# Performance work log

Hardware: AMD Instinct MI355X
Metric: run time of the kernel (lower is better)

## Reference

```python
import jax, jax.numpy as jnp
import numpy as np

B, S, G = 128, 128, 2000          # batch, set_size, n_genes
NH, H, NLAT = 256, 4, 64          # n_hidden, n_heads, n_latent
HD = NH // H                      # head_dim = 64
NGAT = 2                          # n_gat_layers
LN_EPS = 1e-5


def _layer_norm(x, g, b):
    mu = jnp.mean(x, axis=-1, keepdims=True)
    var = jnp.var(x, axis=-1, keepdims=True)
    return (x - mu) * jax.lax.rsqrt(var + LN_EPS) * g + b


def setup_inputs() -> dict:
    key = jax.random.key(0)
    ks = jax.random.split(key, 12)
    x_set = jax.random.normal(ks[0], (B, S, G), dtype=jnp.float32)
    adj = jax.random.randint(ks[1], (B, S, S), 0, 2).astype(jnp.int32)
    # guarantee self-loops so no softmax row is fully masked
    adj = jnp.maximum(adj, jnp.eye(S, dtype=jnp.int32)[None])
    w = 0.02
    return {
        "x_set": x_set,
        "adj": adj,
        "W_in": jax.random.normal(ks[2], (G, NH), dtype=jnp.float32) * w,
        "b_in": jnp.zeros((NH,), jnp.float32),
        "ln_in_g": jnp.ones((NH,), jnp.float32),
        "ln_in_b": jnp.zeros((NH,), jnp.float32),
        "Wg": jax.random.normal(ks[3], (NGAT, NH, NH), dtype=jnp.float32) * w,
        "a_src": jax.random.normal(ks[4], (NGAT, H, HD), dtype=jnp.float32) * 0.1,
        "a_dst": jax.random.normal(ks[5], (NGAT, H, HD), dtype=jnp.float32) * 0.1,
        "a_edge": jax.random.normal(ks[6], (NGAT, H, HD), dtype=jnp.float32) * 0.1,
        "We": jax.random.normal(ks[7], (NGAT, NH, NH), dtype=jnp.float32) * w,
        "ln_g": jnp.ones((NGAT, NH), jnp.float32),
        "ln_b": jnp.zeros((NGAT, NH), jnp.float32),
        "Wz": jax.random.normal(ks[8], (NH, NLAT), dtype=jnp.float32) * w,
        "bz": jnp.zeros((NLAT,), jnp.float32),
    }


def reference(x_set, adj, W_in, b_in, ln_in_g, ln_in_b, Wg, a_src, a_dst,
              a_edge, We, ln_g, ln_b, Wz, bz):
    # input_proj: Linear -> LayerNorm -> GELU (dropout = identity in eval)
    h = jax.nn.gelu(_layer_norm(x_set @ W_in + b_in, ln_in_g, ln_in_b),
                    approximate=False)
    masked = (adj == 0)[..., None]                       # (B,S,S,1)
    for l in range(NGAT):
        hp = (h @ Wg[l]).reshape(B, S, H, HD)            # W(x) per head
        s_src = jnp.einsum('bshd,hd->bsh', hp, a_src[l])
        s_dst = jnp.einsum('bshd,hd->bsh', hp, a_dst[l])
        # edge features e_ij = h_i - h_j; edge_proj is linear (no bias), so
        # <proj(h_i - h_j), a_edge> = es_i - es_j  (exactly the original math,
        # without materializing the (B,S,S,NH) tensor)
        es = jnp.einsum('bshd,hd->bsh', (h @ We[l]).reshape(B, S, H, HD),
                        a_edge[l])
        logits = (s_src + es)[:, :, None, :] + (s_dst - es)[:, None, :, :]
        logits = jnp.where(logits >= 0, logits, 0.2 * logits)  # LeakyReLU(0.2)
        logits = jnp.where(masked, -jnp.inf, logits)
        attn = jax.nn.softmax(logits, axis=2)            # over neighbors j
        out = jnp.einsum('bijh,bjhd->bihd', attn, hp).reshape(B, S, NH)
        h = jax.nn.gelu(_layer_norm(out, ln_g[l], ln_b[l]), approximate=False)
    z_all = h @ Wz + bz                                  # (B,S,NLAT)
    return z_all
```

## Files before the change

### kernel.cpp

```cpp
#include <hip/hip_runtime.h>
#include <hip/hip_bf16.h>
#include <cstdint>
#include <cstddef>

#define BB   128
#define SS   128
#define GG   2000
#define NHID 256
#define NHEAD 4
#define HDIM 64
#define NLAT 64
#define KPAD 2048
#define NSPLIT 4
#define KSPLIT 512

typedef __attribute__((ext_vector_type(4))) float f32x4;
typedef __attribute__((ext_vector_type(8))) short short8;
typedef __attribute__((ext_vector_type(4))) short bfs4;
typedef __attribute__((ext_vector_type(8))) __bf16 bf8_t;

static __device__ __forceinline__ bf8_t as_bf8(short8 s){
  union { short8 s; bf8_t b; } u; u.s = s; return u.b;
}

static __device__ __forceinline__ unsigned short f2bf(float f){
  union { float f; unsigned u; } x; x.f = f;
  unsigned r = x.u + 0x7fffu + ((x.u >> 16) & 1u);
  return (unsigned short)(r >> 16);
}

#define GLOAD_LDS16(g, l) __builtin_amdgcn_global_load_lds( \
    (const __attribute__((address_space(1))) unsigned int*)(g), \
    (__attribute__((address_space(3))) unsigned int*)(l), 16, 0, 0)

__global__ __launch_bounds__(256) void k_transconv(
    const float* __restrict__ W, unsigned short* __restrict__ Wt,
    int K, int N, int Kpad)
{
  int idx = blockIdx.x * 256 + threadIdx.x;
  if (idx >= N * Kpad) return;
  int n = idx / Kpad, k = idx - n * Kpad;
  float v = (k < K) ? W[(size_t)k * N + n] : 0.f;
  Wt[idx] = f2bf(v);
}

__global__ __launch_bounds__(256) void k_adjpack(
    const int* __restrict__ adj, unsigned long long* __restrict__ abits)
{
  const int wid  = blockIdx.x * 4 + (threadIdx.x >> 6);
  const int lane = threadIdx.x & 63;
  int v = adj[(size_t)wid * 64 + lane];
  unsigned long long m = __ballot(v != 0);
  if (lane == 0) abits[wid] = m;
}

__global__ __launch_bounds__(256, 4) void k_gemm_in(
    const float* __restrict__ X,
    const unsigned short* __restrict__ Bt,
    float* __restrict__ Out)
{
  __shared__ __align__(16) unsigned short Ab[2][4][64][8];
  __shared__ __align__(16) unsigned short Bb[2][16][64][8];
  const int tid = threadIdx.x, l = tid & 63, w = tid >> 6;
  const int m0 = blockIdx.x * 64;
  const int kbase = blockIdx.y * KSPLIT;
  const int kvalid = (GG - kbase < KSPLIT) ? (GG - kbase) : KSPLIT;
  const int nsteps = 16;

  const int akg8 = (l >> 4) * 8;
  const float* aP = X + (size_t)(m0 + (l & 15) + 16 * w) * GG + kbase + akg8;
  const unsigned short* bB = Bt + (size_t)(l & 15) * KPAD + kbase + akg8;

  f32x4 acc[4][4];
#pragma unroll
  for (int i = 0; i < 4; ++i)
#pragma unroll
    for (int j = 0; j < 4; ++j) acc[i][j] = (f32x4)(0.f);

  auto stage_b = [&](int buf, int koff) {
#pragma unroll
    for (int q = 0; q < 4; ++q) {
      const int tile = w * 4 + q;
      GLOAD_LDS16(bB + (size_t)(16 * tile) * KPAD + koff, &Bb[buf][tile][0][0]);
    }
  };
  auto load_a = [&](int koff, f32x4& a0, f32x4& a1, bool& ok) {
    ok = (koff + akg8 < kvalid);
    const float* p = ok ? (aP + koff) : (aP - akg8);
    a0 = *(const f32x4*)p;
    a1 = *(const f32x4*)(p + 4);
  };
  auto write_a = [&](int buf, f32x4 a0, f32x4 a1, bool ok) {
    if (!ok) { a0 = (f32x4)(0.f); a1 = (f32x4)(0.f); }
    bf8_t v;
    v[0]=(__bf16)a0.x; v[1]=(__bf16)a0.y; v[2]=(__bf16)a0.z; v[3]=(__bf16)a0.w;
    v[4]=(__bf16)a1.x; v[5]=(__bf16)a1.y; v[6]=(__bf16)a1.z; v[7]=(__bf16)a1.w;
    *(bf8_t*)&Ab[buf][w][l][0] = v;
  };

  {
    f32x4 a0, a1; bool ok;
    load_a(0, a0, a1, ok);
    stage_b(0, 0);
    write_a(0, a0, a1, ok);
  }
  __syncthreads();

  for (int s = 0; s < nsteps; ++s) {
    const int cur = s & 1;
    f32x4 a0, a1; bool ok = false;
    const bool more = (s + 1 < nsteps);
    if (more) {
      load_a((s + 1) * 32, a0, a1, ok);
      stage_b(cur ^ 1, (s + 1) * 32);
    }
    short8 af[4], bfv[4];
#pragma unroll
    for (int i = 0; i < 4; ++i) af[i]  = *(const short8*)&Ab[cur][i][l][0];
#pragma unroll
    for (int j = 0; j < 4; ++j) bfv[j] = *(const short8*)&Bb[cur][4 * w + j][l][0];
#pragma unroll
    for (int i = 0; i < 4; ++i)
#pragma unroll
      for (int j = 0; j < 4; ++j)
        acc[i][j] = __builtin_amdgcn_mfma_f32_16x16x32_bf16(
            as_bf8(af[i]), as_bf8(bfv[j]), acc[i][j], 0, 0, 0);
    if (more) write_a(cur ^ 1, a0, a1, ok);
    __syncthreads();
  }

  float* outp = Out + (size_t)blockIdx.y * ((size_t)BB * SS * NHID);
  const int orow = m0 + ((l >> 4) << 2);
  const int ocol = (w << 6) + (l & 15);
#pragma unroll
  for (int i = 0; i < 4; ++i)
#pragma unroll
    for (int j = 0; j < 4; ++j) {
      const int row = orow + i * 16, col = ocol + j * 16;
#pragma unroll
      for (int r = 0; r < 4; ++r)
        outp[(size_t)(row + r) * NHID + col] = acc[i][j][r];
    }
}

__global__ __launch_bounds__(256, 2) void k_gemm_hp(
    const unsigned short* __restrict__ A,
    const unsigned short* __restrict__ Bt,
    unsigned short* __restrict__ hpT)
{
  __shared__ __align__(16) unsigned short Ab[2][4][64][8];
  __shared__ __align__(16) unsigned short Bb[2][8][64][8];
  const int tid = threadIdx.x, l = tid & 63, w = tid >> 6;
  const int m0 = blockIdx.x * 64, n0 = blockIdx.y * 128;

  const unsigned short* aB = A  + (size_t)(m0 + (l & 15)) * NHID + (l >> 4) * 8;
  const unsigned short* bB = Bt + (size_t)(n0 + (l & 15)) * NHID + (l >> 4) * 8;

  f32x4 acc[4][2];
#pragma unroll
  for (int i = 0; i < 4; ++i)
#pragma unroll
    for (int j = 0; j < 2; ++j) acc[i][j] = (f32x4)(0.f);

  auto stage = [&](int buf, int koff) {
#pragma unroll
    for (int q = 0; q < 3; ++q) {
      const int t = w * 3 + q;
      if (t < 4) {
        GLOAD_LDS16(aB + (size_t)(16 * t) * NHID + koff, &Ab[buf][t][0][0]);
      } else {
        GLOAD_LDS16(bB + (size_t)(16 * (t - 4)) * NHID + koff, &Bb[buf][t - 4][0][0]);
      }
    }
  };

  stage(0, 0);
  __syncthreads();

  for (int s = 0; s < 8; ++s) {
    const int cur = s & 1;
    if (s + 1 < 8) stage(cur ^ 1, (s + 1) * 32);
    short8 af[4], bfv[2];
#pragma unroll
    for (int i = 0; i < 4; ++i) af[i]  = *(const short8*)&Ab[cur][i][l][0];
#pragma unroll
    for (int j = 0; j < 2; ++j) bfv[j] = *(const short8*)&Bb[cur][2 * w + j][l][0];
#pragma unroll
    for (int i = 0; i < 4; ++i)
#pragma unroll
      for (int j = 0; j < 2; ++j)
        acc[i][j] = __builtin_amdgcn_mfma_f32_16x16x32_bf16(
            as_bf8(af[i]), as_bf8(bfv[j]), acc[i][j], 0, 0, 0);
    __syncthreads();
  }

  const int bidx = m0 >> 7;
  const int rb0  = (m0 & 127) + ((l >> 4) << 2);
  unsigned short* hb = hpT + (size_t)bidx * NHID * SS;
#pragma unroll
  for (int i = 0; i < 4; ++i)
#pragma unroll
    for (int j = 0; j < 2; ++j) {
      const int col = n0 + (2 * w + j) * 16 + (l & 15);
      bfs4 o;
#pragma unroll
      for (int r = 0; r < 4; ++r) o[r] = (short)f2bf(acc[i][j][r]);
      *(bfs4*)&hb[(size_t)col * SS + rb0 + i * 16] = o;
    }
}

__global__ __launch_bounds__(256) void k_ln_fuse(
    const float* __restrict__ X0, int nparts, size_t pstride,
    const float* __restrict__ bias, const float* __restrict__ g,
    const float* __restrict__ b, unsigned short* __restrict__ out_bf,
    float* __restrict__ out_f32, const float* __restrict__ u,
    float* __restrict__ c1, float* __restrict__ c2)
{
  const int tid = threadIdx.x, l = tid & 63, w = tid >> 6;
  const f32x4 gg = *(const f32x4*)(g + l * 4);
  const f32x4 bb = *(const f32x4*)(b + l * 4);
  f32x4 bias4 = (f32x4)(0.f);
  if (bias) bias4 = *(const f32x4*)(bias + l * 4);
  f32x4 u1v[4], u2v[4];
  if (u) {
#pragma unroll
    for (int t = 0; t < 4; ++t) {
      u1v[t] = *(const f32x4*)(u + (size_t)(4 * l + t) * 4);
      u2v[t] = *(const f32x4*)(u + 1024 + (size_t)(4 * l + t) * 4);
    }
  }
  for (int it = 0; it < 4; ++it) {
    const int row = blockIdx.x * 16 + w * 4 + it;
    f32x4 x = *(const f32x4*)(X0 + (size_t)row * NHID + l * 4);
    for (int p = 1; p < nparts; ++p) {
      f32x4 x1 = *(const f32x4*)(X0 + p * pstride + (size_t)row * NHID + l * 4);
      x.x += x1.x; x.y += x1.y; x.z += x1.z; x.w += x1.w;
    }
    x.x += bias4.x; x.y += bias4.y; x.z += bias4.z; x.w += bias4.w;
    float s  = x.x + x.y + x.z + x.w;
    float sq = x.x * x.x + x.y * x.y + x.z * x.z + x.w * x.w;
#pragma unroll
    for (int m = 1; m < 64; m <<= 1) { s += __shfl_xor(s, m); sq += __shfl_xor(sq, m); }
    const float mu   = s * (1.f / 256.f);
    const float var  = sq * (1.f / 256.f) - mu * mu;
    const float rstd = rsqrtf(var + 1e-5f);
    float y[4];
#pragma unroll
    for (int t = 0; t < 4; ++t) {
      float yy = (x[t] - mu) * rstd * gg[t] + bb[t];
      y[t] = 0.5f * yy * (1.f + erff(yy * 0.70710678118654752f));
    }
    if (out_bf) {
      bfs4 o;
#pragma unroll
      for (int t = 0; t < 4; ++t) o[t] = (short)f2bf(y[t]);
      *(bfs4*)(out_bf + (size_t)row * NHID + l * 4) = o;
    }
    if (out_f32) {
      f32x4 o; o.x = y[0]; o.y = y[1]; o.z = y[2]; o.w = y[3];
      *(f32x4*)(out_f32 + (size_t)row * NHID + l * 4) = o;
    }
    if (u) {
      float d1[4] = {0.f,0.f,0.f,0.f}, d2[4] = {0.f,0.f,0.f,0.f};
#pragma unroll
      for (int t = 0; t < 4; ++t)
#pragma unroll
        for (int h = 0; h < 4; ++h) {
          d1[h] += y[t] * u1v[t][h];
          d2[h] += y[t] * u2v[t][h];
        }
#pragma unroll
      for (int h = 0; h < 4; ++h) {
#pragma unroll
        for (int m = 1; m < 64; m <<= 1) {
          d1[h] += __shfl_xor(d1[h], m);
          d2[h] += __shfl_xor(d2[h], m);
        }
      }
      if (l == 0) {
#pragma unroll
        for (int h = 0; h < 4; ++h) {
          c1[(size_t)row * 4 + h] = d1[h];
          c2[(size_t)row * 4 + h] = d2[h];
        }
      }
    }
  }
}

__global__ __launch_bounds__(256, 1) void k_proj(
    const float* __restrict__ Wg, const float* __restrict__ We,
    const float* __restrict__ asrc, const float* __restrict__ adst,
    const float* __restrict__ aedge, float* __restrict__ u)
{
  const int lyr = blockIdx.x;
  const int k = threadIdx.x;
  const float* Wgl = Wg + (size_t)lyr * NHID * NHID;
  const float* Wel = We + (size_t)lyr * NHID * NHID;
  float* u1 = u + (size_t)lyr * 2048;
  float* u2 = u1 + 1024;
#pragma unroll
  for (int h = 0; h < 4; ++h) {
    float ss = 0.f, sd = 0.f, se = 0.f;
    const float* wg  = Wgl + k * NHID + h * 64;
    const float* we  = Wel + k * NHID + h * 64;
    const float* pas = asrc + lyr * NHEAD * HDIM + h * 64;
    const float* pad_ = adst + lyr * NHEAD * HDIM + h * 64;
    const float* pae = aedge + lyr * NHEAD * HDIM + h * 64;
#pragma unroll 4
    for (int d = 0; d < 64; ++d) {
      ss += wg[d] * pas[d];
      sd += wg[d] * pad_[d];
      se += we[d] * pae[d];
    }
    u1[k * 4 + h] = ss + se;
    u2[k * 4 + h] = sd - se;
  }
}

__global__ __launch_bounds__(256) void k_attn2(
    const unsigned short* __restrict__ hpT, const float* __restrict__ c1,
    const float* __restrict__ c2, const unsigned long long* __restrict__ abits,
    float* __restrict__ out)
{
  __shared__ __align__(16) unsigned short Pb[4][8][64][8];
  __shared__ __align__(16) unsigned short Vb[4][4][64][8];
  __shared__ float s1[128], s2[128];
  __shared__ float mbuf[2][128], sbuf[2][128], invsum[128];
  const int head = blockIdx.x, b = blockIdx.y;
  const int tid = threadIdx.x, w = tid >> 6, l = tid & 63;

  if (tid < 128) {
    const int m = b * SS + tid;
    s1[tid] = c1[m * 4 + head];
    s2[tid] = c2[m * 4 + head];
  }
  {
    const unsigned short* hb = hpT + ((size_t)b * NHID + head * 64) * SS;
#pragma unroll
    for (int q = 0; q < 4; ++q) {
      const int tile = w * 4 + q;
      const int kstep = tile >> 2, nt = tile & 3;
      const unsigned short* src =
          hb + (size_t)(nt * 16 + (l & 15)) * SS + kstep * 32 + (l >> 4) * 8;
      GLOAD_LDS16(src, &Vb[kstep][nt][0][0]);
    }
  }
  __syncthreads();

  const int i = tid & 127, half = tid >> 7;
  const float s1v = s1[i];
  const unsigned long long bits = abits[((size_t)b * SS + i) * 2 + half];

  float ma[4] = {-3.0e38f, -3.0e38f, -3.0e38f, -3.0e38f};
#pragma unroll
  for (int jl = 0; jl < 64; ++jl) {
    float x  = s1v + s2[half * 64 + jl];
    float lk = fmaxf(x, 0.2f * x);
    float xm = ((bits >> jl) & 1ull) ? lk : -3.0e38f;
    ma[jl & 3] = fmaxf(ma[jl & 3], xm);
  }
  mbuf[half][i] = fmaxf(fmaxf(ma[0], ma[1]), fmaxf(ma[2], ma[3]));
  __syncthreads();
  const float mrow = fmaxf(mbuf[0][i], mbuf[1][i]);

  float sa[4] = {0.f, 0.f, 0.f, 0.f};
#pragma unroll
  for (int grp = 0; grp < 8; ++grp) {
    short8 pv;
#pragma unroll
    for (int e = 0; e < 8; ++e) {
      const int jl = grp * 8 + e;
      float x  = s1v + s2[half * 64 + jl];
      float lk = fmaxf(x, 0.2f * x);
      float xm = ((bits >> jl) & 1ull) ? lk : -3.0e38f;
      float p  = exp2f((xm - mrow) * 1.4426950408889634f);
      sa[e & 3] += p;
      pv[e] = (short)f2bf(p);
    }
    const int j = half * 64 + grp * 8;
    const int kstep = j >> 5, g = (j >> 3) & 3;
    *(short8*)&Pb[kstep][i >> 4][(g << 4) | (i & 15)][0] = pv;
  }
  sbuf[half][i] = (sa[0] + sa[1]) + (sa[2] + sa[3]);
  __syncthreads();
  if (tid < 128) invsum[tid] = 1.f / (sbuf[0][tid] + sbuf[1][tid]);
  __syncthreads();

  f32x4 acc[2][4];
#pragma unroll
  for (int ii = 0; ii < 2; ++ii)
#pragma unroll
    for (int nt = 0; nt < 4; ++nt) acc[ii][nt] = (f32x4)(0.f);
#pragma unroll
  for (int kstep = 0; kstep < 4; ++kstep) {
    short8 bv[4];
#pragma unroll
    for (int nt = 0; nt < 4; ++nt) bv[nt] = *(const short8*)&Vb[kstep][nt][l][0];
#pragma unroll
    for (int ii = 0; ii < 2; ++ii) {
      short8 af = *(const short8*)&Pb[kstep][2 * w + ii][l][0];
#pragma unroll
      for (int nt = 0; nt < 4; ++nt)
        acc[ii][nt] = __builtin_amdgcn_mfma_f32_16x16x32_bf16(
            as_bf8(af), as_bf8(bv[nt]), acc[ii][nt], 0, 0, 0);
    }
  }

  float* ob = out + (size_t)(b * SS) * NHID + head * 64;
#pragma unroll
  for (int ii = 0; ii < 2; ++ii) {
    const int it = 2 * w + ii;
#pragma unroll
    for (int r = 0; r < 4; ++r) {
      const int row = it * 16 + (l >> 4) * 4 + r;
      const float inv = invsum[row];
#pragma unroll
      for (int nt = 0; nt < 4; ++nt)
        ob[(size_t)row * NHID + nt * 16 + (l & 15)] = acc[ii][nt][r] * inv;
    }
  }
}

__global__ __launch_bounds__(256, 1) void k_zgemm(
    const float* __restrict__ hmat, const float* __restrict__ Wz,
    const float* __restrict__ bz, float* __restrict__ Z)
{
  __shared__ __align__(16) float hrows[64 * 256];
  const int tid = threadIdx.x, w = tid >> 6, l = tid & 63;
  const int r0 = blockIdx.x * 64;
  const f32x4* src = (const f32x4*)(hmat + (size_t)r0 * NHID);
#pragma unroll
  for (int rep = 0; rep < 16; ++rep)
    ((f32x4*)hrows)[rep * 256 + tid] = src[rep * 256 + tid];
  __syncthreads();
  const float bzv = bz[l];
  const int rbase = w * 16;
#pragma unroll
  for (int pass = 0; pass < 4; ++pass) {
    float acc0 = 0.f, acc1 = 0.f, acc2 = 0.f, acc3 = 0.f;
    const float* h0 = &hrows[(rbase + pass * 4) * 256];
#pragma unroll 8
    for (int k = 0; k < 256; ++k) {
      float wv = Wz[k * 64 + l];
      acc0 += h0[k] * wv;
      acc1 += h0[256 + k] * wv;
      acc2 += h0[512 + k] * wv;
      acc3 += h0[768 + k] * wv;
    }
    float* zp = Z + (size_t)(r0 + rbase + pass * 4) * 64 + l;
    zp[0]   = acc0 + bzv;
    zp[64]  = acc1 + bzv;
    zp[128] = acc2 + bzv;
    zp[192] = acc3 + bzv;
  }
}

extern "C" void kernel_launch(void* const* d_in, const int* in_sizes, int n_in,
                              void* d_out, int out_size, void* d_ws, size_t ws_size,
                              hipStream_t stream)
{
  const float* x_set   = (const float*)d_in[0];
  const int*   adj     = (const int*)d_in[1];
  const float* W_in    = (const float*)d_in[2];
  const float* b_in    = (const float*)d_in[3];
  const float* ln_in_g = (const float*)d_in[4];
  const float* ln_in_b = (const float*)d_in[5];
  const float* Wg      = (const float*)d_in[6];
  const float* a_src   = (const float*)d_in[7];
  const float* a_dst   = (const float*)d_in[8];
  const float* a_edge  = (const float*)d_in[9];
  const float* We      = (const float*)d_in[10];
  const float* ln_g    = (const float*)d_in[11];
  const float* ln_b    = (const float*)d_in[12];
  const float* Wz      = (const float*)d_in[13];
  const float* bz      = (const float*)d_in[14];
  float* zout = (float*)d_out;

  const int M = BB * SS;
  const size_t PSTRIDE = (size_t)M * NHID;

  char* base = (char*)d_ws;
  size_t off = 0;
  auto alloc = [&](size_t bytes) { char* p = base + off; off += (bytes + 255) & ~(size_t)255; return p; };
  float*          P     = (float*)alloc(PSTRIDE * 4 * NSPLIT);
  unsigned short* hbf   = (unsigned short*)alloc((size_t)M * NHID * 2);
  unsigned short* hpT   = (unsigned short*)alloc((size_t)M * NHID * 2);
  float*          bufA  = (float*)alloc((size_t)M * NHID * 4);
  unsigned short* wt_in = (unsigned short*)alloc((size_t)NHID * KPAD * 2);
  unsigned short* wgt   = (unsigned short*)alloc((size_t)NHID * NHID * 2);
  float*          u     = (float*)alloc(2 * 2048 * 4);
  float*          c1    = (float*)alloc((size_t)M * 4 * 4);
  float*          c2    = (float*)alloc((size_t)M * 4 * 4);
  unsigned long long* abits = (unsigned long long*)alloc((size_t)BB * SS * 2 * 8);
  float* hfin = P;

  k_transconv<<<dim3((NHID * KPAD) / 256), dim3(256), 0, stream>>>(
      W_in, wt_in, GG, NHID, KPAD);
  k_proj<<<dim3(2), dim3(256), 0, stream>>>(Wg, We, a_src, a_dst, a_edge, u);
  k_adjpack<<<dim3(BB * SS * 2 / 4), dim3(256), 0, stream>>>(adj, abits);
  k_gemm_in<<<dim3(M / 64, NSPLIT), dim3(256), 0, stream>>>(x_set, wt_in, P);
  k_ln_fuse<<<dim3(M / 16), dim3(256), 0, stream>>>(
      P, NSPLIT, PSTRIDE, b_in, ln_in_g, ln_in_b, hbf, nullptr,
      u, c1, c2);

  for (int l = 0; l < 2; ++l) {
    const float* Wgl = Wg + (size_t)l * NHID * NHID;
    k_transconv<<<dim3((NHID * NHID) / 256), dim3(256), 0, stream>>>(
        Wgl, wgt, NHID, NHID, NHID);
    k_gemm_hp<<<dim3(M / 64, 2), dim3(256), 0, stream>>>(hbf, wgt, hpT);
    k_attn2<<<dim3(NHEAD, BB), dim3(256), 0, stream>>>(
        hpT, c1, c2, abits, bufA);
    if (l == 0) {
      k_ln_fuse<<<dim3(M / 16), dim3(256), 0, stream>>>(
          bufA, 1, 0, nullptr, ln_g, ln_b, hbf, nullptr,
          u + 2048, c1, c2);
    } else {
      k_ln_fuse<<<dim3(M / 16), dim3(256), 0, stream>>>(
          bufA, 1, 0, nullptr, ln_g + NHID, ln_b + NHID, nullptr, hfin,
          nullptr, nullptr, nullptr);
    }
  }

  k_zgemm<<<dim3(M / 64), dim3(256), 0, stream>>>(hfin, Wz, bz, zout);
}
```

Baseline: 238.0 us.

## Pre-tile X to bf16 MFMA layout and restructure input GEMM split

```diff
diff --git a/kernel.cpp b/kernel.cpp
--- a/kernel.cpp
+++ b/kernel.cpp
@@ -11,8 +11,6 @@
 #define HDIM 64
 #define NLAT 64
 #define KPAD 2048
-#define NSPLIT 4
-#define KSPLIT 512
 
 typedef __attribute__((ext_vector_type(4))) float f32x4;
 typedef __attribute__((ext_vector_type(8))) short short8;
@@ -32,6 +30,39 @@
 #define GLOAD_LDS16(g, l) __builtin_amdgcn_global_load_lds( \
     (const __attribute__((address_space(1))) unsigned int*)(g), \
     (__attribute__((address_space(3))) unsigned int*)(l), 16, 0, 0)
+
+__global__ __launch_bounds__(256) void k_x2tile(
+    const float* __restrict__ X, unsigned short* __restrict__ XT)
+{
+  const int gid = blockIdx.x * 256 + threadIdx.x;
+  const int row = gid >> 8;
+  const int q   = gid & 255;
+  const int k0  = q << 3;
+  short8 v;
+  if (k0 < GG) {
+    f32x4 a0 = *(const f32x4*)(X + (size_t)row * GG + k0);
+    f32x4 a1 = *(const f32x4*)(X + (size_t)row * GG + k0 + 4);
+    v[0]=(short)f2bf(a0.x); v[1]=(short)f2bf(a0.y); v[2]=(short)f2bf(a0.z); v[3]=(short)f2bf(a0.w);
+    v[4]=(short)f2bf(a1.x); v[5]=(short)f2bf(a1.y); v[6]=(short)f2bf(a1.z); v[7]=(short)f2bf(a1.w);
+  } else {
+#pragma unroll
+    for (int t = 0; t < 8; ++t) v[t] = 0;
+  }
+  const int mblk = row >> 5, f = (row >> 4) & 1, ks = q >> 2;
+  const int lane = (row & 15) | ((q & 3) << 4);
+  *(short8*)&XT[(((size_t)(mblk * 64 + ks) * 2 + f) * 64 + lane) * 8] = v;
+}
+
+__global__ __launch_bounds__(256) void k_wtile(
+    const float* __restrict__ W, unsigned short* __restrict__ WT)
+{
+  const int idx = blockIdx.x * 256 + threadIdx.x;
+  const int k = idx >> 8, n = idx & 255;
+  float v = (k < GG) ? W[(size_t)k * NHID + n] : 0.f;
+  const int ks = k >> 5, t = n >> 4;
+  const int lane = (n & 15) | (((k >> 3) & 3) << 4);
+  WT[(((size_t)ks * 16 + t) * 64 + lane) * 8 + (k & 7)] = f2bf(v);
+}
 
 __global__ __launch_bounds__(256) void k_transconv(
     const float* __restrict__ W, unsigned short* __restrict__ Wt,
@@ -54,89 +85,62 @@
   if (lane == 0) abits[wid] = m;
 }
 
-__global__ __launch_bounds__(256, 4) void k_gemm_in(
-    const float* __restrict__ X,
-    const unsigned short* __restrict__ Bt,
-    float* __restrict__ Out)
-{
-  __shared__ __align__(16) unsigned short Ab[2][4][64][8];
+__global__ __launch_bounds__(256, 4) void k_gemm_in2(
+    const unsigned short* __restrict__ XT,
+    const unsigned short* __restrict__ WT,
+    float* __restrict__ Out, size_t pstride)
+{
+  __shared__ __align__(16) unsigned short Ab[2][2][64][8];
   __shared__ __align__(16) unsigned short Bb[2][16][64][8];
   const int tid = threadIdx.x, l = tid & 63, w = tid >> 6;
-  const int m0 = blockIdx.x * 64;
-  const int kbase = blockIdx.y * KSPLIT;
-  const int kvalid = (GG - kbase < KSPLIT) ? (GG - kbase) : KSPLIT;
-  const int nsteps = 16;
-
-  const int akg8 = (l >> 4) * 8;
-  const float* aP = X + (size_t)(m0 + (l & 15) + 16 * w) * GG + kbase + akg8;
-  const unsigned short* bB = Bt + (size_t)(l & 15) * KPAD + kbase + akg8;
-
-  f32x4 acc[4][4];
-#pragma unroll
-  for (int i = 0; i < 4; ++i)
+  const int mblk = blockIdx.x;
+  const int kstep0 = blockIdx.y * 32;
+
+  f32x4 acc[2][4];
+#pragma unroll
+  for (int i = 0; i < 2; ++i)
 #pragma unroll
     for (int j = 0; j < 4; ++j) acc[i][j] = (f32x4)(0.f);
 
-  auto stage_b = [&](int buf, int koff) {
+  auto stage = [&](int buf, int ks) {
 #pragma unroll
     for (int q = 0; q < 4; ++q) {
-      const int tile = w * 4 + q;
-      GLOAD_LDS16(bB + (size_t)(16 * tile) * KPAD + koff, &Bb[buf][tile][0][0]);
-    }
+      const int t = 4 * w + q;
+      GLOAD_LDS16(WT + ((size_t)ks * 16 + t) * 512 + l * 8, &Bb[buf][t][0][0]);
+    }
+    if (w < 2)
+      GLOAD_LDS16(XT + (((size_t)mblk * 64 + ks) * 2 + w) * 512 + l * 8,
+                  &Ab[buf][w][0][0]);
   };
-  auto load_a = [&](int koff, f32x4& a0, f32x4& a1, bool& ok) {
-    ok = (koff + akg8 < kvalid);
-    const float* p = ok ? (aP + koff) : (aP - akg8);
-    a0 = *(const f32x4*)p;
-    a1 = *(const f32x4*)(p + 4);
-  };
-  auto write_a = [&](int buf, f32x4 a0, f32x4 a1, bool ok) {
-    if (!ok) { a0 = (f32x4)(0.f); a1 = (f32x4)(0.f); }
-    bf8_t v;
-    v[0]=(__bf16)a0.x; v[1]=(__bf16)a0.y; v[2]=(__bf16)a0.z; v[3]=(__bf16)a0.w;
-    v[4]=(__bf16)a1.x; v[5]=(__bf16)a1.y; v[6]=(__bf16)a1.z; v[7]=(__bf16)a1.w;
-    *(bf8_t*)&Ab[buf][w][l][0] = v;
-  };
-
-  {
-    f32x4 a0, a1; bool ok;
-    load_a(0, a0, a1, ok);
-    stage_b(0, 0);
-    write_a(0, a0, a1, ok);
-  }
-  __syncthreads();
-
-  for (int s = 0; s < nsteps; ++s) {
+
+  stage(0, kstep0);
+  __syncthreads();
+
+  for (int s = 0; s < 32; ++s) {
     const int cur = s & 1;
-    f32x4 a0, a1; bool ok = false;
-    const bool more = (s + 1 < nsteps);
-    if (more) {
-      load_a((s + 1) * 32, a0, a1, ok);
-      stage_b(cur ^ 1, (s + 1) * 32);
-    }
-    short8 af[4], bfv[4];
-#pragma unroll
-    for (int i = 0; i < 4; ++i) af[i]  = *(const short8*)&Ab[cur][i][l][0];
+    if (s + 1 < 32) stage(cur ^ 1, kstep0 + s + 1);
+    short8 af[2], bfv[4];
+#pragma unroll
+    for (int i = 0; i < 2; ++i) af[i]  = *(const short8*)&Ab[cur][i][l][0];
 #pragma unroll
     for (int j = 0; j < 4; ++j) bfv[j] = *(const short8*)&Bb[cur][4 * w + j][l][0];
 #pragma unroll
-    for (int i = 0; i < 4; ++i)
+    for (int i = 0; i < 2; ++i)
 #pragma unroll
       for (int j = 0; j < 4; ++j)
         acc[i][j] = __builtin_amdgcn_mfma_f32_16x16x32_bf16(
             as_bf8(af[i]), as_bf8(bfv[j]), acc[i][j], 0, 0, 0);
-    if (more) write_a(cur ^ 1, a0, a1, ok);
     __syncthreads();
   }
 
-  float* outp = Out + (size_t)blockIdx.y * ((size_t)BB * SS * NHID);
-  const int orow = m0 + ((l >> 4) << 2);
-  const int ocol = (w << 6) + (l & 15);
-#pragma unroll
-  for (int i = 0; i < 4; ++i)
+  float* outp = Out + (size_t)blockIdx.y * pstride;
+  const int orow0 = mblk * 32 + ((l >> 4) << 2);
+  const int ocol  = (w << 6) + (l & 15);
+#pragma unroll
+  for (int i = 0; i < 2; ++i)
 #pragma unroll
     for (int j = 0; j < 4; ++j) {
-      const int row = orow + i * 16, col = ocol + j * 16;
+      const int row = orow0 + i * 16, col = ocol + j * 16;
 #pragma unroll
       for (int r = 0; r < 4; ++r)
         outp[(size_t)(row + r) * NHID + col] = acc[i][j][r];
@@ -483,7 +487,8 @@
   char* base = (char*)d_ws;
   size_t off = 0;
   auto alloc = [&](size_t bytes) { char* p = base + off; off += (bytes + 255) & ~(size_t)255; return p; };
-  float*          P     = (float*)alloc(PSTRIDE * 4 * NSPLIT);
+  unsigned short* XT    = (unsigned short*)alloc((size_t)M * KPAD * 2);
+  float*          P     = (float*)alloc(PSTRIDE * 4 * 2);
   unsigned short* hbf   = (unsigned short*)alloc((size_t)M * NHID * 2);
   unsigned short* hpT   = (unsigned short*)alloc((size_t)M * NHID * 2);
   float*          bufA  = (float*)alloc((size_t)M * NHID * 4);
@@ -495,13 +500,13 @@
   unsigned long long* abits = (unsigned long long*)alloc((size_t)BB * SS * 2 * 8);
   float* hfin = P;
 
-  k_transconv<<<dim3((NHID * KPAD) / 256), dim3(256), 0, stream>>>(
-      W_in, wt_in, GG, NHID, KPAD);
+  k_wtile<<<dim3((NHID * KPAD) / 256), dim3(256), 0, stream>>>(W_in, wt_in);
+  k_x2tile<<<dim3((M * (KPAD / 8)) / 256), dim3(256), 0, stream>>>(x_set, XT);
   k_proj<<<dim3(2), dim3(256), 0, stream>>>(Wg, We, a_src, a_dst, a_edge, u);
   k_adjpack<<<dim3(BB * SS * 2 / 4), dim3(256), 0, stream>>>(adj, abits);
-  k_gemm_in<<<dim3(M / 64, NSPLIT), dim3(256), 0, stream>>>(x_set, wt_in, P);
+  k_gemm_in2<<<dim3(M / 32, 2), dim3(256), 0, stream>>>(XT, wt_in, P, PSTRIDE);
   k_ln_fuse<<<dim3(M / 16), dim3(256), 0, stream>>>(
-      P, NSPLIT, PSTRIDE, b_in, ln_in_g, ln_in_b, hbf, nullptr,
+      P, 2, PSTRIDE, b_in, ln_in_g, ln_in_b, hbf, nullptr,
       u, c1, c2);
 
   for (int l = 0; l < 2; ++l) {
```

Measured after the change: 266.1 us. 11.8% more time.
